# Kernel optimization log

Measured on AMD Instinct MI355X. Metric: run time of the kernel, lower is better.

## Reference

```python
import jax, jax.numpy as jnp
import numpy as np

DIM = 1024
NUM_ATT = 8
NUM_HEADS = 16
HEAD_DIM = DIM // NUM_HEADS
ROPE_BASE = 10000.0
NEG_INF = -1e9


def _rope(x):
    # x: [B, H, L, hd]; torchtune-style interleaved RoPE applied along the sequence axis.
    B, H, L, hd = x.shape
    pos = jnp.arange(L, dtype=jnp.float32)
    inv_freq = 1.0 / (ROPE_BASE ** (jnp.arange(0, hd, 2, dtype=jnp.float32) / hd))
    ang = pos[:, None] * inv_freq[None, :]          # [L, hd/2]
    cos = jnp.cos(ang)[None, None]                  # [1,1,L,hd/2]
    sin = jnp.sin(ang)[None, None]
    xr = x.reshape(B, H, L, hd // 2, 2)
    x0, x1 = xr[..., 0], xr[..., 1]
    out = jnp.stack([x0 * cos - x1 * sin, x1 * cos + x0 * sin], axis=-1)
    return out.reshape(B, H, L, hd).astype(x.dtype)


def setup_inputs() -> dict:
    key = jax.random.key(0)
    ks = jax.random.split(key, 7)
    B, L = 32, 512
    x = jax.random.normal(ks[0], (B, L, DIM), dtype=jnp.float32)
    s = 0.02  # init scale for numerical sanity (init choice, not math)
    query_projs = jax.random.normal(ks[1], (NUM_ATT, DIM, DIM), dtype=jnp.float32) * s
    key_projs = jax.random.normal(ks[2], (NUM_ATT, DIM, DIM), dtype=jnp.float32) * s
    value_projs = jax.random.normal(ks[3], (NUM_ATT, DIM, DIM), dtype=jnp.float32) * s
    out_projs = jax.random.normal(ks[4], (NUM_ATT, DIM, DIM), dtype=jnp.float32) * s
    router_w = jax.random.normal(ks[5], (DIM, NUM_ATT), dtype=jnp.float32) * s
    router_b = jnp.zeros((NUM_ATT,), dtype=jnp.float32)
    return {"x": x, "query_projs": query_projs, "key_projs": key_projs,
            "value_projs": value_projs, "out_projs": out_projs,
            "router_w": router_w, "router_b": router_b}


def reference(x, query_projs, key_projs, value_projs, out_projs, router_w, router_b):
    B, L, D = x.shape
    H, hd = NUM_HEADS, HEAD_DIM
    scale = hd ** -0.5

    # top-1 routing on mean-pooled tokens
    logits = x.mean(axis=1) @ router_w + router_b       # [B, E]
    attn_probs = jax.nn.softmax(logits, axis=-1)
    routes = jnp.argmax(attn_probs, axis=-1)            # [B] int

    # per-batch weight gather (the memory-bound irregular access) + bmm
    qw = query_projs[routes]                             # [B, D, D]
    kw = key_projs[routes]
    vw = value_projs[routes]
    q = jnp.einsum('bld,bde->ble', x, qw)
    k = jnp.einsum('bld,bde->ble', x, kw)
    v = jnp.einsum('bld,bde->ble', x, vw)

    q = q.reshape(B, L, H, hd).transpose(0, 2, 1, 3)     # [B,H,L,hd]
    k = k.reshape(B, L, H, hd).transpose(0, 2, 1, 3)
    v = v.reshape(B, L, H, hd).transpose(0, 2, 1, 3)

    q = _rope(q)
    k = _rope(k)

    scores = jnp.einsum('bhld,bhmd->bhlm', q, k) * scale  # [B,H,L,L]
    causal = jnp.triu(jnp.ones((L, L), dtype=bool), k=1)  # True above diag = masked
    scores = jnp.where(causal[None, None], NEG_INF, scores)
    attn = jax.nn.softmax(scores, axis=-1)
    out = jnp.einsum('bhlm,bhmd->bhld', attn, v)          # [B,H,L,hd]
    out = out.transpose(0, 2, 1, 3).reshape(B, L, D)

    ow = out_projs[routes]                                # [B, D, D]
    out = jnp.einsum('bld,bde->ble', out, ow)
    return out, attn_probs
```

## Files before the change

kernel.cpp:

```cpp
#include <hip/hip_runtime.h>


typedef __attribute__((ext_vector_type(8))) short bf16x8;
typedef __attribute__((ext_vector_type(4))) float f32x4;

typedef const __attribute__((address_space(1))) unsigned short* gas_t;
typedef __attribute__((address_space(3))) unsigned short* las_t;

#define OFF_PART   (0ull)
#define OFF_ROUTES (2ull << 20)
#define OFF_XB     (3ull << 20)
#define OFF_WT     (40ull << 20)
#define OFF_QKV    (112ull << 20)

__device__ __forceinline__ unsigned short f2bf(float f){
  unsigned int u = __float_as_uint(f);
  u += 0x7fffu + ((u >> 16) & 1u);
  return (unsigned short)(u >> 16);
}


__global__ void meanpool_kernel(const float* __restrict__ x, float* __restrict__ part,
                                unsigned short* __restrict__ xb){
  const int b = blockIdx.x, lc = blockIdx.y, t = threadIdx.x;
  const size_t base = ((size_t)b*512 + lc*32)*1024;
  const float* xs = x + base;
  unsigned short* xo = xb + base;
  float a0=0.f, a1=0.f, a2=0.f, a3=0.f;
  for (int l = 0; l < 32; ++l){
    const float* row = xs + l*1024;
    unsigned short* orow = xo + l*1024;
    const float v0 = row[t], v1 = row[t+256], v2 = row[t+512], v3 = row[t+768];
    a0 += v0; a1 += v1; a2 += v2; a3 += v3;
    orow[t] = f2bf(v0); orow[t+256] = f2bf(v1); orow[t+512] = f2bf(v2); orow[t+768] = f2bf(v3);
  }
  float* o = part + ((size_t)b*16 + lc)*1024;
  o[t] = a0; o[t+256] = a1; o[t+512] = a2; o[t+768] = a3;
}

__global__ void router_kernel(const float* __restrict__ part,
                              const float* __restrict__ rw,
                              const float* __restrict__ rbias,
                              float* __restrict__ probs,
                              int* __restrict__ routes){
  const int b = blockIdx.x, t = threadIdx.x;
  __shared__ float xbar[1024];
  __shared__ float red[256*8];
  #pragma unroll
  for (int k = 0; k < 4; ++k){
    const int d = t + k*256;
    float s = 0.f;
    for (int lc = 0; lc < 16; ++lc) s += part[((size_t)b*16 + lc)*1024 + d];
    xbar[d] = s * (1.0f/512.0f);
  }
  __syncthreads();
  float p[8] = {0.f,0.f,0.f,0.f,0.f,0.f,0.f,0.f};
  #pragma unroll
  for (int k = 0; k < 4; ++k){
    const int d = t + k*256;
    const float xv = xbar[d];
    #pragma unroll
    for (int e = 0; e < 8; ++e) p[e] = fmaf(xv, rw[d*8 + e], p[e]);
  }
  #pragma unroll
  for (int e = 0; e < 8; ++e) red[t*8 + e] = p[e];
  __syncthreads();
  for (int s2 = 128; s2 > 0; s2 >>= 1){
    if (t < s2){
      #pragma unroll
      for (int e = 0; e < 8; ++e) red[t*8 + e] += red[(t + s2)*8 + e];
    }
    __syncthreads();
  }
  if (t == 0){
    float lg[8], mx = -3e38f; int am = 0;
    #pragma unroll
    for (int e = 0; e < 8; ++e){
      lg[e] = red[e] + rbias[e];
      if (lg[e] > mx){ mx = lg[e]; am = e; }
    }
    float sum = 0.f, ex[8];
    #pragma unroll
    for (int e = 0; e < 8; ++e){ ex[e] = __expf(lg[e] - mx); sum += ex[e]; }
    const float inv = 1.0f / sum;
    #pragma unroll
    for (int e = 0; e < 8; ++e) probs[b*8 + e] = ex[e] * inv;
    routes[b] = am;
  }
}


__global__ void wcast_kernel(const float* __restrict__ W, unsigned short* __restrict__ Wt){
  __shared__ float tile[32][33];
  const int mtx = blockIdx.z;
  const float* Wm = W + (size_t)mtx*1024*1024;
  unsigned short* Wo = Wt + (size_t)mtx*1024*1024;
  const int t = threadIdx.x;
  const int c = t & 31, r0 = t >> 5;
  const int gx = blockIdx.x*32, gy = blockIdx.y*32;
  #pragma unroll
  for (int k = 0; k < 4; ++k){
    const int r = r0 + k*8;
    tile[r][c] = Wm[(size_t)(gy + r)*1024 + gx + c];
  }
  __syncthreads();
  #pragma unroll
  for (int k = 0; k < 4; ++k){
    const int r = r0 + k*8;
    Wo[(size_t)(gx + r)*1024 + gy + c] = f2bf(tile[c][r]);
  }
}


template<int MODE>
__global__ __launch_bounds__(256, 2) void gemm_kernel(
    const unsigned short* __restrict__ A,
    const unsigned short* __restrict__ Wt,
    const int* __restrict__ routes,
    unsigned short* __restrict__ qkvout,
    float* __restrict__ outf)
{
  __shared__ __align__(16) unsigned short As[2][128*32];
  __shared__ __align__(16) unsigned short Bs[2][128*32];

  int wg = blockIdx.x + (blockIdx.y << 3) + (blockIdx.z << 5);
  wg = (wg & 7) * ((MODE == 0) ? 384 : 128) + (wg >> 3);
  const int z   = wg >> 5;
  const int rem = wg & 31;
  const int m0  = (rem >> 3) * 128;
  const int n0  = (rem & 7) * 128;
  const int b = (MODE == 0) ? (z / 3) : z;
  const int p = (MODE == 0) ? (z - b*3) : 0;

  const int route = routes[b];
  const unsigned short* Ab = A + (size_t)b*512*1024;
  const unsigned short* Wb = Wt + (size_t)((MODE == 0) ? (p*8 + route) : route)*1024*1024;
  const int t = threadIdx.x;
  const int lane = t & 63;
  const int wave = t >> 6;
  const int wm = (wave >> 1) * 64;
  const int wn = (wave & 1) * 64;
  const int quad = lane >> 4;
  const int ln = lane & 15;

  f32x4 acc[4][4] = {};

  const int u0 = t, u1 = t + 256;
  const int r0s = u0 >> 2, c0s = (u0 & 3) ^ ((r0s >> 1) & 3);
  const int r1s = u1 >> 2, c1s = (u1 & 3) ^ ((r1s >> 1) & 3);
  const unsigned short* gA0 = Ab + (size_t)(m0 + r0s)*1024 + c0s*8;
  const unsigned short* gA1 = Ab + (size_t)(m0 + r1s)*1024 + c1s*8;
  const unsigned short* gB0 = Wb + (size_t)(n0 + r0s)*1024 + c0s*8;
  const unsigned short* gB1 = Wb + (size_t)(n0 + r1s)*1024 + c1s*8;
  las_t lA0 = (las_t)(&As[0][0] + u0*8), lA1 = (las_t)(&As[0][0] + u1*8);
  las_t lB0 = (las_t)(&Bs[0][0] + u0*8), lB1 = (las_t)(&Bs[0][0] + u1*8);

  const int swz = (quad ^ ((ln >> 1) & 3)) * 8;
  int offA[4], offB[4];
  #pragma unroll
  for (int i = 0; i < 4; ++i){
    offA[i] = (wm + i*16 + ln)*32 + swz;
    offB[i] = (wn + i*16 + ln)*32 + swz;
  }

#define STAGE(buf, kk) do { \
    const int boff_ = (buf)*4096; \
    __builtin_amdgcn_global_load_lds((gas_t)(gA0 + (kk)), lA0 + boff_, 16, 0, 0); \
    __builtin_amdgcn_global_load_lds((gas_t)(gA1 + (kk)), lA1 + boff_, 16, 0, 0); \
    __builtin_amdgcn_global_load_lds((gas_t)(gB0 + (kk)), lB0 + boff_, 16, 0, 0); \
    __builtin_amdgcn_global_load_lds((gas_t)(gB1 + (kk)), lB1 + boff_, 16, 0, 0); \
  } while (0)

  STAGE(0, 0);
  for (int k0 = 0; k0 < 1024; k0 += 32){
    const int cur = (k0 >> 5) & 1;
    __syncthreads();
    if (k0 + 32 < 1024) STAGE(cur ^ 1, k0 + 32);
    const unsigned short* Al = &As[cur][0];
    const unsigned short* Bl = &Bs[cur][0];
    bf16x8 av[4], bv[4];
    #pragma unroll
    for (int i = 0; i < 4; ++i){
      av[i] = *(const bf16x8*)(Al + offA[i]);
      bv[i] = *(const bf16x8*)(Bl + offB[i]);
    }
    #pragma unroll
    for (int i = 0; i < 4; ++i)
      #pragma unroll
      for (int j = 0; j < 4; ++j)
        acc[i][j] = __builtin_amdgcn_mfma_f32_16x16x32_bf16(av[i], bv[j], acc[i][j], 0, 0, 0);
  }
#undef STAGE

  if (MODE == 0){
    const size_t PSZ = (size_t)32*16*512*64;
    if (p < 2){
      #pragma unroll
      for (int j = 0; j < 4; ++j){
        const int e  = n0 + wn + j*16 + ln;
        const int h  = e >> 6;
        const int eh = e & 63;
        const float invf = exp2f(-0.41524101f * (float)(eh >> 1));
        float s1, c1; __sincosf(invf, &s1, &c1);
        unsigned short* outp = qkvout + ((((size_t)p*32 + b)*16 + h)*512)*64 + eh;
        const int l0 = m0 + wm + quad*4;
        #pragma unroll
        for (int i = 0; i < 4; ++i){
          float sn, cs;
          __sincosf((float)(l0 + i*16) * invf, &sn, &cs);
          #pragma unroll
          for (int r = 0; r < 4; ++r){
            const int l = l0 + i*16 + r;
            const float own = acc[i][j][r];
            const float par = __shfl_xor(own, 1, 64);
            const float v = (e & 1) ? fmaf(own, cs, par*sn) : fmaf(own, cs, -par*sn);
            outp[(size_t)l*64] = f2bf(v);
            const float nc = cs*c1 - sn*s1;
            const float ns = sn*c1 + cs*s1;
            cs = nc; sn = ns;
          }
        }
      }
    } else {
      #pragma unroll
      for (int j = 0; j < 4; ++j){
        const int e  = n0 + wn + j*16 + ln;
        const int h  = e >> 6;
        const int eh = e & 63;
        unsigned short* outp = qkvout + 2*PSZ + (((size_t)b*16 + h)*64 + eh)*512;
        #pragma unroll
        for (int i = 0; i < 4; ++i){
          const int l0 = m0 + wm + i*16 + quad*4;
          ushort4 pk;
          pk.x = f2bf(acc[i][j][0]); pk.y = f2bf(acc[i][j][1]);
          pk.z = f2bf(acc[i][j][2]); pk.w = f2bf(acc[i][j][3]);
          *(ushort4*)(outp + l0) = pk;
        }
      }
    }
  } else {
    #pragma unroll
    for (int j = 0; j < 4; ++j){
      const int e = n0 + wn + j*16 + ln;
      #pragma unroll
      for (int i = 0; i < 4; ++i){
        #pragma unroll
        for (int r = 0; r < 4; ++r){
          const int l = m0 + wm + i*16 + quad*4 + r;
          outf[((size_t)b*512 + l)*1024 + e] = acc[i][j][r];
        }
      }
    }
  }
}


#define PSTR 72

__global__ __launch_bounds__(256, 3) void attn_kernel(
    const unsigned short* __restrict__ qkv,
    unsigned short* __restrict__ ctx)
{
  __shared__ __align__(16) unsigned short Ks[2][64*64];
  __shared__ __align__(16) unsigned short Vts[2][64*64];
  __shared__ __align__(16) unsigned short Ps[4][32*PSTR];

  int wg = blockIdx.x + (blockIdx.y << 2) + (blockIdx.z << 6);
  wg = (wg & 7) * 256 + (wg >> 3);
  const int b  = wg >> 6;
  const int h  = (wg >> 2) & 15;
  const int qt = wg & 3;

  const size_t HO  = (((size_t)b)*16 + h)*512*64;
  const size_t PSZ = (size_t)32*16*512*64;
  const unsigned short* Qg  = qkv + HO;
  const unsigned short* Kg  = qkv + PSZ + HO;
  const unsigned short* Vtg = qkv + 2*PSZ + HO;

  const int t    = threadIdx.x;
  const int lane = t & 63;
  const int wave = t >> 6;
  const int quad = lane >> 4;
  const int ln   = lane & 15;

  const int u0 = t, u1 = t + 256;
  const int kr0 = u0 >> 3, kc0 = (u0 & 7) ^ (kr0 & 7);
  const int kr1 = u1 >> 3, kc1 = (u1 & 7) ^ (kr1 & 7);

  bf16x8 aq[2][2];
  #pragma unroll
  for (int rg = 0; rg < 2; ++rg){
    const int row = qt*128 + rg*64 + wave*16 + ln;
    #pragma unroll
    for (int ks = 0; ks < 2; ++ks)
      aq[rg][ks] = *(const bf16x8*)(Qg + (size_t)row*64 + ks*32 + quad*8);
  }

  const int ktEnd = 2*qt + 1;

  __builtin_amdgcn_global_load_lds((gas_t)(Kg  + kr0*64  + kc0*8), (las_t)(Ks[0]  + u0*8), 16,0,0);
  __builtin_amdgcn_global_load_lds((gas_t)(Kg  + kr1*64  + kc1*8), (las_t)(Ks[0]  + u1*8), 16,0,0);
  __builtin_amdgcn_global_load_lds((gas_t)(Vtg + kr0*512 + kc0*8), (las_t)(Vts[0] + u0*8), 16,0,0);
  __builtin_amdgcn_global_load_lds((gas_t)(Vtg + kr1*512 + kc1*8), (las_t)(Vts[0] + u1*8), 16,0,0);

  float m_r[2][4], l_r[2][4];
  #pragma unroll
  for (int rg = 0; rg < 2; ++rg)
    #pragma unroll
    for (int r = 0; r < 4; ++r){ m_r[rg][r] = -3e38f; l_r[rg][r] = 0.f; }
  f32x4 o[2][4] = {};

  const int swzl = ln & 7;
  unsigned short* Pw = Ps[wave];
  const int rowoff = wave*16 + quad*4;

  for (int kt = 0; kt <= ktEnd; ++kt){
    __syncthreads();
    if (kt < ktEnd){
      const unsigned short* Kn  = Kg + (kt+1)*4096;
      const int col = (kt+1)*64;
      unsigned short* kb = Ks[(kt+1)&1];
      unsigned short* vb = Vts[(kt+1)&1];
      __builtin_amdgcn_global_load_lds((gas_t)(Kn  + kr0*64 + kc0*8),        (las_t)(kb + u0*8), 16,0,0);
      __builtin_amdgcn_global_load_lds((gas_t)(Kn  + kr1*64 + kc1*8),        (las_t)(kb + u1*8), 16,0,0);
      __builtin_amdgcn_global_load_lds((gas_t)(Vtg + kr0*512 + col + kc0*8), (las_t)(vb + u0*8), 16,0,0);
      __builtin_amdgcn_global_load_lds((gas_t)(Vtg + kr1*512 + col + kc1*8), (las_t)(vb + u1*8), 16,0,0);
    }
    const unsigned short* ks_ = Ks[kt&1];
    const unsigned short* vt_ = Vts[kt&1];

    #pragma unroll
    for (int rg = 0; rg < 2; ++rg){
      if (rg == 0 && kt > 2*qt) continue;
      const bool diag = (kt == 2*qt + rg);

      f32x4 s[4] = {};
      __builtin_amdgcn_s_setprio(1);
      #pragma unroll
      for (int ks2 = 0; ks2 < 2; ++ks2){
        #pragma unroll
        for (int kn = 0; kn < 4; ++kn){
          const bf16x8 bk = *(const bf16x8*)(ks_ + (kn*16+ln)*64 + (((quad + ks2*4) ^ swzl))*8);
          s[kn] = __builtin_amdgcn_mfma_f32_16x16x32_bf16(aq[rg][ks2], bk, s[kn], 0, 0, 0);
        }
      }
      __builtin_amdgcn_s_setprio(0);

      float p[4][4], lm[4] = {-3e38f,-3e38f,-3e38f,-3e38f};
      #pragma unroll
      for (int kn = 0; kn < 4; ++kn){
        const int col = kn*16 + ln;
        #pragma unroll
        for (int r = 0; r < 4; ++r){
          float v = s[kn][r] * 0.125f;
          if (diag && col > rowoff + r) v = -1e9f;
          p[kn][r] = v;
          lm[r] = fmaxf(lm[r], v);
        }
      }
      #pragma unroll
      for (int off = 1; off < 16; off <<= 1)
        #pragma unroll
        for (int r = 0; r < 4; ++r)
          lm[r] = fmaxf(lm[r], __shfl_xor(lm[r], off, 64));
      float alpha[4], rsum[4];
      #pragma unroll
      for (int r = 0; r < 4; ++r){
        const float mn = fmaxf(m_r[rg][r], lm[r]);
        alpha[r] = __expf(m_r[rg][r] - mn);
        m_r[rg][r] = mn;
      }
      #pragma unroll
      for (int kn = 0; kn < 4; ++kn)
        #pragma unroll
        for (int r = 0; r < 4; ++r)
          p[kn][r] = __expf(p[kn][r] - m_r[rg][r]);
      #pragma unroll
      for (int r = 0; r < 4; ++r)
        rsum[r] = (p[0][r] + p[1][r]) + (p[2][r] + p[3][r]);
      #pragma unroll
      for (int off = 1; off < 16; off <<= 1)
        #pragma unroll
        for (int r = 0; r < 4; ++r)
          rsum[r] += __shfl_xor(rsum[r], off, 64);
      #pragma unroll
      for (int r = 0; r < 4; ++r) l_r[rg][r] = l_r[rg][r]*alpha[r] + rsum[r];
      #pragma unroll
      for (int dn = 0; dn < 4; ++dn)
        #pragma unroll
        for (int r = 0; r < 4; ++r)
          o[rg][dn][r] *= alpha[r];

      #pragma unroll
      for (int kn = 0; kn < 4; ++kn)
        #pragma unroll
        for (int r = 0; r < 4; ++r)
          Pw[(rg*16 + quad*4 + r)*PSTR + kn*16 + ln] = f2bf(p[kn][r]);

      __builtin_amdgcn_s_setprio(1);
      #pragma unroll
      for (int ks2 = 0; ks2 < 2; ++ks2){
        const bf16x8 ap = *(const bf16x8*)(Pw + (rg*16 + ln)*PSTR + quad*8 + ks2*32);
        #pragma unroll
        for (int dn = 0; dn < 4; ++dn){
          const bf16x8 bv = *(const bf16x8*)(vt_ + (dn*16+ln)*64 + (((quad + ks2*4) ^ swzl))*8);
          o[rg][dn] = __builtin_amdgcn_mfma_f32_16x16x32_bf16(ap, bv, o[rg][dn], 0, 0, 0);
        }
      }
      __builtin_amdgcn_s_setprio(0);
    }
  }

  #pragma unroll
  for (int rg = 0; rg < 2; ++rg){
    #pragma unroll
    for (int r = 0; r < 4; ++r){
      const float inv = 1.0f / l_r[rg][r];
      const int row = qt*128 + rg*64 + wave*16 + quad*4 + r;
      unsigned short* op = ctx + ((size_t)b*512 + row)*1024 + h*64 + ln;
      #pragma unroll
      for (int dn = 0; dn < 4; ++dn)
        op[dn*16] = f2bf(o[rg][dn][r] * inv);
    }
  }
}


extern "C" void kernel_launch(void* const* d_in, const int* in_sizes, int n_in,
                              void* d_out, int out_size, void* d_ws, size_t ws_size,
                              hipStream_t stream) {
  const float* x     = (const float*)d_in[0];
  const float* qw    = (const float*)d_in[1];
  const float* kw    = (const float*)d_in[2];
  const float* vw    = (const float*)d_in[3];
  const float* ow    = (const float*)d_in[4];
  const float* rw    = (const float*)d_in[5];
  const float* rbias = (const float*)d_in[6];
  float* out = (float*)d_out;
  char* ws = (char*)d_ws;

  float* part            = (float*)(ws + OFF_PART);
  int* routes            = (int*)(ws + OFF_ROUTES);
  unsigned short* xb     = (unsigned short*)(ws + OFF_XB);
  unsigned short* wt     = (unsigned short*)(ws + OFF_WT);
  unsigned short* qkvbuf = (unsigned short*)(ws + OFF_QKV);
  unsigned short* ctx    = xb;
  float* probs = out + (size_t)32*512*1024;

  meanpool_kernel<<<dim3(32, 16), 256, 0, stream>>>(x, part, xb);
  router_kernel<<<32, 256, 0, stream>>>(part, rw, rbias, probs, routes);
  wcast_kernel<<<dim3(32, 32, 8), 256, 0, stream>>>(qw, wt);
  wcast_kernel<<<dim3(32, 32, 8), 256, 0, stream>>>(kw, wt + (size_t)8*1024*1024);
  wcast_kernel<<<dim3(32, 32, 8), 256, 0, stream>>>(vw, wt + (size_t)16*1024*1024);
  wcast_kernel<<<dim3(32, 32, 8), 256, 0, stream>>>(ow, wt + (size_t)24*1024*1024);
  gemm_kernel<0><<<dim3(8, 4, 96), 256, 0, stream>>>(xb, wt, routes, qkvbuf, nullptr);
  attn_kernel<<<dim3(4, 16, 32), 256, 0, stream>>>(qkvbuf, ctx);
  gemm_kernel<1><<<dim3(8, 4, 32), 256, 0, stream>>>(ctx, wt + (size_t)24*1024*1024, routes,
                                                     nullptr, out);
}
```

Measured before the change: 516.1 us.

## Triple-buffer GEMM LDS tiles with partial vmcnt waits and MFMA priority boost

Moves the projection GEMM main loop from double to triple buffering in LDS. Each iteration now waits only until the previous stage's global-to-LDS loads have landed (vmcnt(4)) instead of a full __syncthreads, so two stages of loads stay in flight during compute. It also raises wave priority around the MFMA block with s_setprio. LDS use grows by half, which may lower occupancy under launch_bounds(256,2), and the hand-written waitcnt and barrier sequence must stay correct across the three buffers.

```diff
diff --git a/kernel.cpp b/kernel.cpp
--- a/kernel.cpp
+++ b/kernel.cpp
@@ -120,8 +120,8 @@
     unsigned short* __restrict__ qkvout,
     float* __restrict__ outf)
 {
-  __shared__ __align__(16) unsigned short As[2][128*32];
-  __shared__ __align__(16) unsigned short Bs[2][128*32];
+  __shared__ __align__(16) unsigned short As[3][128*32];
+  __shared__ __align__(16) unsigned short Bs[3][128*32];
 
   int wg = blockIdx.x + (blockIdx.y << 3) + (blockIdx.z << 5);
   wg = (wg & 7) * ((MODE == 0) ? 384 : 128) + (wg >> 3);
@@ -164,33 +164,50 @@
   }
 
 #define STAGE(buf, kk) do { \
-    const int boff_ = (buf)*4096; \
-    __builtin_amdgcn_global_load_lds((gas_t)(gA0 + (kk)), lA0 + boff_, 16, 0, 0); \
-    __builtin_amdgcn_global_load_lds((gas_t)(gA1 + (kk)), lA1 + boff_, 16, 0, 0); \
-    __builtin_amdgcn_global_load_lds((gas_t)(gB0 + (kk)), lB0 + boff_, 16, 0, 0); \
-    __builtin_amdgcn_global_load_lds((gas_t)(gB1 + (kk)), lB1 + boff_, 16, 0, 0); \
+    const int bo_ = (buf)*4096; \
+    __builtin_amdgcn_global_load_lds((gas_t)(gA0 + (kk)), lA0 + bo_, 16, 0, 0); \
+    __builtin_amdgcn_global_load_lds((gas_t)(gA1 + (kk)), lA1 + bo_, 16, 0, 0); \
+    __builtin_amdgcn_global_load_lds((gas_t)(gB0 + (kk)), lB0 + bo_, 16, 0, 0); \
+    __builtin_amdgcn_global_load_lds((gas_t)(gB1 + (kk)), lB1 + bo_, 16, 0, 0); \
   } while (0)
 
+#define COMPUTE(buf) do { \
+    const unsigned short* Al_ = &As[buf][0]; \
+    const unsigned short* Bl_ = &Bs[buf][0]; \
+    bf16x8 av[4], bv[4]; \
+    _Pragma("unroll") \
+    for (int i = 0; i < 4; ++i){ \
+      av[i] = *(const bf16x8*)(Al_ + offA[i]); \
+      bv[i] = *(const bf16x8*)(Bl_ + offB[i]); \
+    } \
+    __builtin_amdgcn_s_setprio(1); \
+    _Pragma("unroll") \
+    for (int i = 0; i < 4; ++i) \
+      _Pragma("unroll") \
+      for (int j = 0; j < 4; ++j) \
+        acc[i][j] = __builtin_amdgcn_mfma_f32_16x16x32_bf16(av[i], bv[j], acc[i][j], 0, 0, 0); \
+    __builtin_amdgcn_s_setprio(0); \
+  } while (0)
+
   STAGE(0, 0);
-  for (int k0 = 0; k0 < 1024; k0 += 32){
-    const int cur = (k0 >> 5) & 1;
-    __syncthreads();
-    if (k0 + 32 < 1024) STAGE(cur ^ 1, k0 + 32);
-    const unsigned short* Al = &As[cur][0];
-    const unsigned short* Bl = &Bs[cur][0];
-    bf16x8 av[4], bv[4];
-    #pragma unroll
-    for (int i = 0; i < 4; ++i){
-      av[i] = *(const bf16x8*)(Al + offA[i]);
-      bv[i] = *(const bf16x8*)(Bl + offB[i]);
-    }
-    #pragma unroll
-    for (int i = 0; i < 4; ++i)
-      #pragma unroll
-      for (int j = 0; j < 4; ++j)
-        acc[i][j] = __builtin_amdgcn_mfma_f32_16x16x32_bf16(av[i], bv[j], acc[i][j], 0, 0, 0);
-  }
+  STAGE(1, 32);
+  for (int t8 = 0; t8 < 30; ++t8){
+    asm volatile("s_waitcnt vmcnt(4)" ::: "memory");
+    __builtin_amdgcn_s_barrier();
+    __builtin_amdgcn_sched_barrier(0);
+    STAGE((t8 + 2) % 3, t8*32 + 64);
+    COMPUTE(t8 % 3);
+  }
+  asm volatile("s_waitcnt vmcnt(4)" ::: "memory");
+  __builtin_amdgcn_s_barrier();
+  __builtin_amdgcn_sched_barrier(0);
+  COMPUTE(0);
+  asm volatile("s_waitcnt vmcnt(0)" ::: "memory");
+  __builtin_amdgcn_s_barrier();
+  __builtin_amdgcn_sched_barrier(0);
+  COMPUTE(1);
 #undef STAGE
+#undef COMPUTE
 
   if (MODE == 0){
     const size_t PSZ = (size_t)32*16*512*64;
```

Result: no change. 523.9 us (+1.5%).
